# Kernel optimization log

Hardware: AMD Instinct MI355X
Metric: run time of the kernel (lower is better)

The kernel has to match this reference:

```python
import jax, jax.numpy as jnp
import numpy as np
import math

N_NODES = 50000
N_EDGES = 800000
IN_DIM = 128
HID = 128
OUT_DIM = 2048
N_LABEL_EDGES = 4096
POOL_RATIO = 0.5
NUM_HEADS = 8


def seg_sum(x, idx, n):
    return jax.ops.segment_sum(x, idx, num_segments=n)


def graph_conv(x, W, b, src, dst, emask, n):
    # DGL GraphConv, norm='both': D_out^-1/2 A D_in^-1/2 (x W) + b (masked edges)
    deg_out = seg_sum(emask, src, n)
    deg_in = seg_sum(emask, dst, n)
    ns = jax.lax.rsqrt(jnp.maximum(deg_out, 1.0))
    nd = jax.lax.rsqrt(jnp.maximum(deg_in, 1.0))
    h = x @ W
    msg = (h * ns[:, None])[src] * emask[:, None]
    agg = seg_sum(msg, dst, n)
    return agg * nd[:, None] + b


def conv_pool_block(x, src, dst, emask, cW, cb, sW, sb):
    # GraphConv -> ReLU -> SAGPool(top-k by GraphConv score, tanh gate) -> avg||max readout
    n = x.shape[0]
    h = jax.nn.relu(graph_conv(x, cW, cb, src, dst, emask, n))
    score = graph_conv(h, sW, sb, src, dst, emask, n)[:, 0]
    k = int(math.ceil(POOL_RATIO * n))  # static
    _, perm = jax.lax.top_k(score, k)
    h_new = h[perm] * jnp.tanh(score[perm])[:, None]
    # remap edges to the pooled node set; drop edges touching removed nodes via mask
    newid = jnp.full((n,), -1, jnp.int32).at[perm].set(jnp.arange(k, dtype=jnp.int32))
    nsrc = newid[src]
    ndst = newid[dst]
    new_mask = emask * (nsrc >= 0).astype(emask.dtype) * (ndst >= 0).astype(emask.dtype)
    nsrc = jnp.maximum(nsrc, 0)
    ndst = jnp.maximum(ndst, 0)
    readout = jnp.concatenate([h_new.mean(0), h_new.max(0)])[None, :]  # [1, 2*HID]
    return h_new, nsrc, ndst, new_mask, readout


def gat_conv(x, fcW, al, ar, lsrc, ldst, n, slope=0.2):
    # GATConv(1 -> 1, num_heads=8): head feature dim is 1
    h = x @ fcW                      # [n, heads]
    el = h * al
    er = h * ar
    e = jax.nn.leaky_relu(el[lsrc] + er[ldst], slope)  # [E_l, heads]
    emax = jax.ops.segment_max(e, ldst, num_segments=n)
    emax = jnp.where(jnp.isfinite(emax), emax, 0.0)
    ex = jnp.exp(e - emax[ldst])
    denom = seg_sum(ex, ldst, n)
    alpha = ex / jnp.maximum(denom[ldst], 1e-9)
    out = seg_sum(alpha * h[lsrc], ldst, n)            # [n, heads]
    return out[:, :, None]                             # [n, heads, 1]


def setup_inputs() -> dict:
    key = jax.random.key(0)
    ks = jax.random.split(key, 32)

    def rn(k, shape, s=0.05):
        return jax.random.normal(k, shape, jnp.float32) * s

    inp = {}
    inp['feat'] = jax.random.normal(ks[0], (N_NODES, IN_DIM), jnp.float32)
    inp['sequence_feature'] = jax.random.normal(ks[1], (1, 1024), jnp.float32)
    inp['src'] = jax.random.randint(ks[2], (N_EDGES,), 0, N_NODES, jnp.int32)
    inp['dst'] = jax.random.randint(ks[3], (N_EDGES,), 0, N_NODES, jnp.int32)
    inp['label_src'] = jax.random.randint(ks[4], (N_LABEL_EDGES,), 0, OUT_DIM, jnp.int32)
    inp['label_dst'] = jax.random.randint(ks[5], (N_LABEL_EDGES,), 0, OUT_DIM, jnp.int32)
    i = 6
    for b in range(3):
        din = IN_DIM if b == 0 else HID
        inp['cW%d' % b] = rn(ks[i], (din, HID)); i += 1
        inp['cb%d' % b] = jnp.zeros((HID,), jnp.float32)
        inp['sW%d' % b] = rn(ks[i], (HID, 1)); i += 1
        inp['sb%d' % b] = jnp.zeros((1,), jnp.float32)
    inp['lin1W'] = rn(ks[i], (2 * HID + 1024, 2 * HID)); i += 1
    inp['lin1b'] = jnp.zeros((2 * HID,), jnp.float32)
    inp['lin2W'] = rn(ks[i], (2 * HID, HID)); i += 1
    inp['lin2b'] = jnp.zeros((HID,), jnp.float32)
    inp['lin3W'] = rn(ks[i], (HID, OUT_DIM)); i += 1
    inp['lin3b'] = jnp.zeros((OUT_DIM,), jnp.float32)
    inp['gat_fcW'] = rn(ks[i], (1, NUM_HEADS)); i += 1
    inp['gat_al'] = rn(ks[i], (NUM_HEADS,)); i += 1
    inp['gat_ar'] = rn(ks[i], (NUM_HEADS,)); i += 1
    return inp


def reference(feat, sequence_feature, src, dst, label_src, label_dst,
              cW0, cb0, sW0, sb0, cW1, cb1, sW1, sb1, cW2, cb2, sW2, sb2,
              lin1W, lin1b, lin2W, lin2b, lin3W, lin3b,
              gat_fcW, gat_al, gat_ar):
    x, s, d = feat, src, dst
    emask = jnp.ones((src.shape[0],), jnp.float32)
    final = None
    for cW, cb, sW, sb in ((cW0, cb0, sW0, sb0), (cW1, cb1, sW1, sb1), (cW2, cb2, sW2, sb2)):
        x, s, d, emask, ro = conv_pool_block(x, s, d, emask, cW, cb, sW, sb)
        final = ro if final is None else final + ro
    final = jnp.concatenate([final, sequence_feature], axis=-1)  # [1, 2*HID+1024]
    f = jax.nn.relu(final @ lin1W + lin1b)
    # dropout: eval mode -> identity
    f = jax.nn.relu(f @ lin2W + lin2b)
    f = f @ lin3W + lin3b          # [1, OUT_DIM]
    ft = f.T                       # [OUT_DIM, 1]
    gat_out = gat_conv(ft, gat_fcW, gat_al, gat_ar, label_src, label_dst, OUT_DIM)
    max_value = jnp.max(gat_out, axis=1)      # [OUT_DIM, 1]
    _ = ft - jax.nn.relu(max_value)           # computed then discarded, as in source
    return ft.T
```

## Files before the change

kernel.cpp:

```cpp
#include <hip/hip_runtime.h>
#include <hip/hip_bf16.h>
#include <cmath>

#define N0 50000
#define NEDGE 800000
#define NEG_HUGE -3.402823466e38f
#define BMAX 64
#define STRIDE 128

typedef int i32x4 __attribute__((ext_vector_type(4)));
typedef __attribute__((ext_vector_type(8))) short short8v;
typedef __attribute__((ext_vector_type(4))) float f32x4;

__device__ inline float b2f(unsigned short u) { return __uint_as_float(((unsigned)u) << 16); }

__device__ inline unsigned short f2b(float f) {
    __hip_bfloat16 h = __float2bfloat16(f);
    return *(unsigned short*)&h;
}

__device__ inline unsigned fkey(float f) {
    unsigned b = __float_as_uint(f);
    if (b == 0x80000000u) b = 0u;
    return (b & 0x80000000u) ? ~b : (b | 0x80000000u);
}

__device__ inline void atomicMaxF(float* a, float v) {
    if (v >= 0.f) atomicMax((int*)a, __float_as_int(v));
    else          atomicMin((unsigned int*)a, __float_as_uint(v));
}

__global__ void k_init(float* finalv, float* f1raw, int* deg_out, int* fill,
                       int* binsA, int* binsB, float* maxbuf, int* ctrl) {
    int i = blockIdx.x * blockDim.x + threadIdx.x;
    if (i < 256) { finalv[i] = 0.f; f1raw[i] = 0.f; }
    if (i < 384) maxbuf[i] = NEG_HUGE;
    if (i < N0) { deg_out[i] = 0; fill[i] = 0; }
    if (i < 65536) { binsA[i] = 0; binsB[i] = 0; }
    if (i < 2) ctrl[8 + i] = 0;
}

__global__ __launch_bounds__(256) void k_build(
        const int* __restrict__ esrc, const int* __restrict__ edst,
        int* deg_out, int* fill, int* csr_src) {
    int t = blockIdx.x * 256 + threadIdx.x;
    int e0 = t * 4;
    if (e0 >= NEDGE) return;
    i32x4 a = __builtin_nontemporal_load((const i32x4*)(esrc + e0));
    i32x4 bq = __builtin_nontemporal_load((const i32x4*)(edst + e0));
    int s[4] = {a.x, a.y, a.z, a.w};
    int d[4] = {bq.x, bq.y, bq.z, bq.w};
#pragma unroll
    for (int kq = 0; kq < 4; ++kq) {
        atomicAdd(&deg_out[s[kq]], 1);
        int pos = atomicAdd(&fill[d[kq]], 1);
        if (pos < STRIDE) csr_src[(size_t)d[kq] * STRIDE + pos] = s[kq];
    }
}

__global__ __launch_bounds__(256) void k_rmbuild(
        const int* __restrict__ esrc, const int* __restrict__ edst,
        const int2* __restrict__ ein, int use_pair,
        const int* __restrict__ ctrl, int slot,
        const int* __restrict__ newid,
        int2* __restrict__ eout, int* __restrict__ outcnt,
        int* deg_out, int* fill, int* csr_src) {
    __shared__ int wbase[4];
    __shared__ int blkbase;
    int E = (slot < 0) ? NEDGE : ctrl[slot];
    if (blockIdx.x * 256 >= E) return;
    int i = blockIdx.x * 256 + threadIdx.x;
    int lane = threadIdx.x & 63, w = threadIdx.x >> 6;
    int ns = -1, nd = -1;
    if (i < E) {
        int s, d;
        if (use_pair) { int2 pr = ein[i]; s = pr.x; d = pr.y; }
        else { s = esrc[i]; d = edst[i]; }
        ns = newid[s]; nd = newid[d];
    }
    bool keep = (ns >= 0) && (nd >= 0);
    unsigned long long m = __ballot(keep);
    int rank = __popcll(m & ((1ull << lane) - 1ull));
    if (lane == 0) wbase[w] = __popcll(m);
    __syncthreads();
    if (threadIdx.x == 0)
        blkbase = atomicAdd(outcnt, wbase[0] + wbase[1] + wbase[2] + wbase[3]);
    __syncthreads();
    int base = blkbase;
    for (int q = 0; q < w; ++q) base += wbase[q];
    if (keep) {
        eout[base + rank] = make_int2(ns, nd);
        atomicAdd(&deg_out[ns], 1);
        int pos = atomicAdd(&fill[nd], 1);
        if (pos < STRIDE) csr_src[(size_t)nd * STRIDE + pos] = ns;
    }
}

__global__ __launch_bounds__(256) void k_gemm(
        const float* __restrict__ feat, const float* __restrict__ xprev,
        const int* __restrict__ oldid, const float* __restrict__ garr,
        const int* __restrict__ deg_out,
        const float* __restrict__ W, unsigned short* __restrict__ hpre,
        int n, int nprev, int mode) {
    __shared__ short Wt[128][136];
    __shared__ short Xt[64][136];
    __shared__ int ridx_s[64];
    __shared__ float esc_s[64];
    int tid = threadIdx.x;
    int r0 = blockIdx.x * 64;
    if (tid < 64) {
        int gr = r0 + tid;
        int ridx = 0; float esc = 0.f;
        if (gr < n) {
            if (mode == 0) {
                ridx = gr;
                esc = rsqrtf(fmaxf((float)deg_out[gr], 1.f));
            } else {
                int orow = oldid[gr];
                if ((unsigned)orow < (unsigned)nprev) {
                    ridx = orow;
                    esc = rsqrtf(fmaxf((float)deg_out[gr], 1.f)) * garr[gr];
                }
            }
        }
        ridx_s[tid] = ridx;
        esc_s[tid] = esc;
    }
    __syncthreads();
    {
        int col = tid & 127;
        int kh = tid >> 7;
#pragma unroll
        for (int c8 = 0; c8 < 8; ++c8) {
            int kb = kh * 64 + c8 * 8;
            unsigned short v[8];
#pragma unroll
            for (int j = 0; j < 8; ++j)
                v[j] = f2b(W[(size_t)(kb + j) * 128 + col]);
            *(uint4*)&Wt[col][kb] = *(uint4*)v;
        }
    }
    {
        const float* xsrc = (mode == 0) ? feat : xprev;
        int rr = tid >> 2;
        int kx = (tid & 3) * 32;
        const float4* xp = (const float4*)(xsrc + (size_t)ridx_s[rr] * 128 + kx);
#pragma unroll
        for (int c4 = 0; c4 < 8; ++c4) {
            float4 v = xp[c4];
            unsigned short u[4];
            u[0] = f2b(v.x); u[1] = f2b(v.y); u[2] = f2b(v.z); u[3] = f2b(v.w);
            *(uint2*)&Xt[rr][kx + c4 * 4] = *(uint2*)u;
        }
    }
    __syncthreads();

    int lane = tid & 63, w = tid >> 6;
    int row16 = lane & 15;
    int ko = (lane >> 4) * 8;
    f32x4 acc[8];
#pragma unroll
    for (int t = 0; t < 8; ++t) acc[t] = (f32x4){0.f, 0.f, 0.f, 0.f};
#pragma unroll
    for (int kc = 0; kc < 4; ++kc) {
        int kbase = kc * 32 + ko;
        short8v a = *(short8v*)&Xt[w * 16 + row16][kbase];
#pragma unroll
        for (int t = 0; t < 8; ++t) {
            short8v b = *(short8v*)&Wt[t * 16 + row16][kbase];
            acc[t] = __builtin_amdgcn_mfma_f32_16x16x32_bf16(a, b, acc[t], 0, 0, 0);
        }
    }
    int rq = (lane >> 4) * 4;
    float esc[4];
#pragma unroll
    for (int r = 0; r < 4; ++r) esc[r] = esc_s[w * 16 + rq + r];
#pragma unroll
    for (int r = 0; r < 4; ++r) {
        int gr = r0 + w * 16 + rq + r;
        if (gr < n) {
            unsigned short* op = hpre + (size_t)gr * 128;
#pragma unroll
            for (int t = 0; t < 8; ++t)
                op[t * 16 + (lane & 15)] = f2b(acc[t][r] * esc[r]);
        }
    }
}

__global__ __launch_bounds__(256) void k_agg_conv(
        const unsigned short* __restrict__ hpre, const int* __restrict__ fill,
        const int* __restrict__ deg_out,
        const int* __restrict__ csr_src,
        const float* __restrict__ cb, const float* __restrict__ sW,
        float* __restrict__ hpost, float* __restrict__ hs, int n) {
    int wid = threadIdx.x >> 6;
    int lane = threadIdx.x & 63;
    int d = blockIdx.x * 4 + wid;
    if (d >= n) return;
    int degin = fill[d];
    int cnt = min(degin, STRIDE);
    const int* bp = csr_src + (size_t)d * STRIDE;
    float a0 = 0.f, a1 = 0.f;
    int j = 0;
    for (; j + 8 <= cnt; j += 8) {
        int4 s0 = *(const int4*)(bp + j);
        int4 s1 = *(const int4*)(bp + j + 4);
        ushort2 u0 = ((const ushort2*)(hpre + (size_t)s0.x * 128))[lane];
        ushort2 u1 = ((const ushort2*)(hpre + (size_t)s0.y * 128))[lane];
        ushort2 u2 = ((const ushort2*)(hpre + (size_t)s0.z * 128))[lane];
        ushort2 u3 = ((const ushort2*)(hpre + (size_t)s0.w * 128))[lane];
        ushort2 u4 = ((const ushort2*)(hpre + (size_t)s1.x * 128))[lane];
        ushort2 u5 = ((const ushort2*)(hpre + (size_t)s1.y * 128))[lane];
        ushort2 u6 = ((const ushort2*)(hpre + (size_t)s1.z * 128))[lane];
        ushort2 u7 = ((const ushort2*)(hpre + (size_t)s1.w * 128))[lane];
        a0 += ((b2f(u0.x) + b2f(u1.x)) + (b2f(u2.x) + b2f(u3.x))) +
              ((b2f(u4.x) + b2f(u5.x)) + (b2f(u6.x) + b2f(u7.x)));
        a1 += ((b2f(u0.y) + b2f(u1.y)) + (b2f(u2.y) + b2f(u3.y))) +
              ((b2f(u4.y) + b2f(u5.y)) + (b2f(u6.y) + b2f(u7.y)));
    }
    for (; j + 4 <= cnt; j += 4) {
        int4 ss = *(const int4*)(bp + j);
        ushort2 u0 = ((const ushort2*)(hpre + (size_t)ss.x * 128))[lane];
        ushort2 u1 = ((const ushort2*)(hpre + (size_t)ss.y * 128))[lane];
        ushort2 u2 = ((const ushort2*)(hpre + (size_t)ss.z * 128))[lane];
        ushort2 u3 = ((const ushort2*)(hpre + (size_t)ss.w * 128))[lane];
        a0 += (b2f(u0.x) + b2f(u1.x)) + (b2f(u2.x) + b2f(u3.x));
        a1 += (b2f(u0.y) + b2f(u1.y)) + (b2f(u2.y) + b2f(u3.y));
    }
    for (; j < cnt; ++j) {
        int s0 = bp[j];
        ushort2 u0 = ((const ushort2*)(hpre + (size_t)s0 * 128))[lane];
        a0 += b2f(u0.x);
        a1 += b2f(u0.y);
    }
    float nd2 = rsqrtf(fmaxf((float)degin, 1.f));
    int c0 = lane * 2;
    float h0 = fmaxf(fmaf(a0, nd2, cb[c0]), 0.f);
    float h1 = fmaxf(fmaf(a1, nd2, cb[c0 + 1]), 0.f);
    ((float2*)(hpost + (size_t)d * 128))[lane] = make_float2(h0, h1);
    float v = h0 * sW[c0] + h1 * sW[c0 + 1];
#pragma unroll
    for (int off = 32; off; off >>= 1) v += __shfl_down(v, off);
    if (lane == 0) hs[d] = v * rsqrtf(fmaxf((float)deg_out[d], 1.f));
}

__global__ void k_score_hist(const float* __restrict__ hs, const int* __restrict__ fill,
                             const int* __restrict__ csr_src,
                             const float* __restrict__ sb, float* score,
                             int* binsA, int n) {
    int d = blockIdx.x * blockDim.x + threadIdx.x;
    if (d >= n) return;
    int degin = fill[d];
    int cnt = min(degin, STRIDE);
    const int* bp = csr_src + (size_t)d * STRIDE;
    float sum = 0.f;
    int j = 0;
    for (; j + 8 <= cnt; j += 8) {
        int4 s0 = *(const int4*)(bp + j);
        int4 s1 = *(const int4*)(bp + j + 4);
        sum += ((hs[s0.x] + hs[s0.y]) + (hs[s0.z] + hs[s0.w])) +
               ((hs[s1.x] + hs[s1.y]) + (hs[s1.z] + hs[s1.w]));
    }
    for (; j + 4 <= cnt; j += 4) {
        int4 ss = *(const int4*)(bp + j);
        sum += (hs[ss.x] + hs[ss.y]) + (hs[ss.z] + hs[ss.w]);
    }
    for (; j < cnt; ++j) sum += hs[bp[j]];
    float sc = rsqrtf(fmaxf((float)degin, 1.f)) * sum + sb[0];
    score[d] = sc;
    atomicAdd(&binsA[fkey(sc) >> 16], 1);
}

__global__ void k_rhist2(const float* __restrict__ score, const int* __restrict__ ctrl,
                         int n, int* binsB) {
    unsigned p16 = (unsigned)ctrl[3];
    for (int i = blockIdx.x * 256 + threadIdx.x; i < n; i += gridDim.x * 256) {
        unsigned u = fkey(score[i]);
        if ((u >> 16) == p16) atomicAdd(&binsB[u & 0xFFFFu], 1);
    }
}

__global__ void k_rpick(int stage, int k0, int* ctrl, const int* __restrict__ bins) {
    __shared__ int gs[64];
    __shared__ int arr[1024];
    __shared__ int wsum[16];
    __shared__ int sChunk, sKrem;
    int t = threadIdx.x;
    {
        int c = t >> 4, sub = t & 15;
        const int4* p4 = (const int4*)(bins + (size_t)c * 1024);
        int s = 0;
#pragma unroll
        for (int q = 0; q < 16; ++q) {
            int4 v = p4[q * 16 + sub];
            s += v.x + v.y + v.z + v.w;
        }
#pragma unroll
        for (int off = 8; off; off >>= 1) s += __shfl_down(s, off, 16);
        if (sub == 0) gs[c] = s;
    }
    __syncthreads();
    if (t == 0) {
        int kneed = (stage == 0) ? k0 : ctrl[4];
        int cum = 0, c = 63;
        for (; c >= 1; --c) { int v = gs[c]; if (cum + v >= kneed) break; cum += v; }
        sChunk = c; sKrem = kneed - cum;
    }
    __syncthreads();
    int c = sChunk;
    int v = bins[(size_t)c * 1024 + t];
    arr[t] = v;
    int lane = t & 63, w = t >> 6;
    int s = v;
#pragma unroll
    for (int off = 32; off; off >>= 1) s += __shfl_down(s, off);
    if (lane == 0) wsum[w] = s;
    __syncthreads();
    if (t == 0) {
        int kneed = sKrem;
        int cum = 0, w2 = 15;
        for (; w2 >= 1; --w2) { int vv = wsum[w2]; if (cum + vv >= kneed) break; cum += vv; }
        int j = 63;
        for (; j >= 1; --j) { int vv = arr[w2 * 64 + j]; if (cum + vv >= kneed) break; cum += vv; }
        int bin = c * 1024 + w2 * 64 + j;
        if (stage == 0) { ctrl[3] = bin; ctrl[4] = kneed - cum; }
        else {
            ctrl[0] = (int)((((unsigned)ctrl[3]) << 16) | (unsigned)bin);
            ctrl[2] = kneed - cum;
        }
    }
}

__global__ void k_ccnt(const float* __restrict__ score, const int* __restrict__ ctrl,
                       int n, int* cntG, int* cntE) {
    __shared__ int wG[16], wE[16];
    int b = blockIdx.x;
    int i = b * 1024 + threadIdx.x;
    int lane = threadIdx.x & 63, wid = threadIdx.x >> 6;
    unsigned T = (unsigned)ctrl[0];
    bool inb = (i < n);
    unsigned u = inb ? fkey(score[i]) : 0u;
    bool isG = inb && (u > T);
    bool isE = inb && (u == T);
    unsigned long long mG = __ballot(isG);
    unsigned long long mE = __ballot(isE);
    if (lane == 0) { wG[wid] = __popcll(mG); wE[wid] = __popcll(mE); }
    __syncthreads();
    if (threadIdx.x == 0) {
        int sg = 0, se = 0;
#pragma unroll
        for (int w = 0; w < 16; ++w) { sg += wG[w]; se += wE[w]; }
        cntG[b] = sg; cntE[b] = se;
    }
}

__global__ void k_cemit(const float* __restrict__ score, const int* __restrict__ ctrl,
                        const int* __restrict__ cntG, const int* __restrict__ cntE,
                        int n, int knext, int* newid, int* oldid, float* garr,
                        int* deg_out, int* fill, int* binsA, int* binsB) {
    __shared__ int wG[16], wE[16];
    __shared__ int sGoff, sEoff;
    int b = blockIdx.x;
    int i = b * 1024 + threadIdx.x;
    if (knext > 0) {
        for (int z = i; z < 65536; z += gridDim.x * 1024) { binsA[z] = 0; binsB[z] = 0; }
        if (i < knext) { deg_out[i] = 0; fill[i] = 0; }
    }
    int lane = threadIdx.x & 63, wid = threadIdx.x >> 6;
    unsigned T = (unsigned)ctrl[0];
    int needEq = ctrl[2];
    bool inb = (i < n);
    float sc = inb ? score[i] : 0.f;
    unsigned u = inb ? fkey(sc) : 0u;
    bool isG = inb && (u > T);
    bool isE = inb && (u == T);
    unsigned long long mG = __ballot(isG);
    unsigned long long mE = __ballot(isE);
    if (lane == 0) { wG[wid] = __popcll(mG); wE[wid] = __popcll(mE); }
    if (threadIdx.x < 64) {
        int l = threadIdx.x;
        int vg = (l < b) ? cntG[l] : 0;
        int ve = (l < b) ? cntE[l] : 0;
#pragma unroll
        for (int off2 = 32; off2; off2 >>= 1) {
            vg += __shfl_down(vg, off2);
            ve += __shfl_down(ve, off2);
        }
        if (l == 0) { sGoff = vg; sEoff = ve; }
    }
    __syncthreads();
    unsigned long long below = (1ull << lane) - 1ull;
    int gW = 0, eW = 0;
    for (int w = 0; w < wid; ++w) { gW += wG[w]; eW += wE[w]; }
    int Gb = sGoff + gW + __popcll(mG & below);
    int Eb = sEoff + eW + __popcll(mE & below);
    if (inb) {
        bool sel = isG || (isE && (Eb < needEq));
        if (sel) {
            int j = Gb + min(Eb, needEq);
            newid[i] = j;
            oldid[j] = i;
            garr[j] = tanhf(sc);
        } else {
            newid[i] = -1;
        }
    }
}

__global__ void k_readout(const float* __restrict__ hpost, const int* __restrict__ oldid,
                          const float* __restrict__ garr, float* finalv, float* maxbuf,
                          int k, int n, float invk) {
    int c = threadIdx.x;
    float sum = 0.f, mx = NEG_HUGE;
    for (int r = blockIdx.x; r < k; r += gridDim.x) {
        int o = oldid[r];
        if ((unsigned)o >= (unsigned)n) continue;
        float g = garr[r];
        float v = hpost[(size_t)o * 128 + c] * g;
        sum += v;
        mx = fmaxf(mx, v);
    }
    atomicAdd(&finalv[c], sum * invk);
    atomicMaxF(&maxbuf[c], mx);
}

__global__ void k_mlp1(const float* __restrict__ finalv, const float* __restrict__ maxbuf,
                       const float* __restrict__ seq, const float* __restrict__ W1,
                       float* f1raw) {
    int o = threadIdx.x;
    int j0 = blockIdx.x * 128;
    float acc = 0.f;
    for (int jj = 0; jj < 128; ++jj) {
        int j = j0 + jj;
        float fv;
        if (j < 128) fv = finalv[j];
        else if (j < 256) fv = maxbuf[j - 128] + maxbuf[j] + maxbuf[j + 128];
        else fv = seq[j - 256];
        acc = fmaf(fv, W1[(size_t)j * 256 + o], acc);
    }
    atomicAdd(&f1raw[o], acc);
}

__global__ void k_mlp2(const float* __restrict__ f1raw, const float* __restrict__ b1,
                       const float* __restrict__ W2, const float* __restrict__ bb2,
                       float* f2v) {
    __shared__ float f1s[256];
    int t = threadIdx.x;
    f1s[t] = fmaxf(f1raw[t] + b1[t], 0.f);
    f1s[t + 128] = fmaxf(f1raw[t + 128] + b1[t + 128], 0.f);
    __syncthreads();
    float acc = 0.f;
    for (int j = 0; j < 256; ++j)
        acc = fmaf(f1s[j], W2[(size_t)j * 128 + t], acc);
    f2v[t] = fmaxf(acc + bb2[t], 0.f);
}

__global__ void k_mlp3(const float* __restrict__ f2v, const float* __restrict__ W3,
                       const float* __restrict__ b3, float* out) {
    __shared__ float f2s[128];
    int t = threadIdx.x;
    f2s[t] = f2v[t];
    __syncthreads();
    int col = blockIdx.x * 128 + t;
    float acc = 0.f;
    for (int j = 0; j < 128; ++j)
        acc = fmaf(f2s[j], W3[(size_t)j * 2048 + col], acc);
    out[col] = acc + b3[col];
}

extern "C" void kernel_launch(void* const* d_in, const int* in_sizes, int n_in,
                              void* d_out, int out_size, void* d_ws, size_t ws_size,
                              hipStream_t stream) {
    (void)in_sizes; (void)n_in; (void)out_size; (void)ws_size;
    const float* feat = (const float*)d_in[0];
    const float* seq  = (const float*)d_in[1];
    const int* src = (const int*)d_in[2];
    const int* dst = (const int*)d_in[3];
    const float *cW[3], *cb[3], *sW[3], *sb[3];
    for (int b = 0; b < 3; ++b) {
        cW[b] = (const float*)d_in[6 + 4 * b];
        cb[b] = (const float*)d_in[7 + 4 * b];
        sW[b] = (const float*)d_in[8 + 4 * b];
        sb[b] = (const float*)d_in[9 + 4 * b];
    }
    const float* lin1W = (const float*)d_in[18];
    const float* lin1b = (const float*)d_in[19];
    const float* lin2W = (const float*)d_in[20];
    const float* lin2b = (const float*)d_in[21];
    const float* lin3W = (const float*)d_in[22];
    const float* lin3b = (const float*)d_in[23];
    float* out = (float*)d_out;

    char* p = (char*)d_ws;
    size_t off = 0;
    auto alloc = [&](size_t bytes) -> void* {
        void* r = p + off;
        off = (off + bytes + 255) & ~(size_t)255;
        return r;
    };
    unsigned short* hpre = (unsigned short*)alloc((size_t)N0 * 128 * 2);
    float* hpost  = (float*)alloc((size_t)N0 * 128 * 4);
    float* hs     = (float*)alloc((size_t)N0 * 4);
    float* score  = (float*)alloc((size_t)N0 * 4);
    int* deg_out  = (int*)alloc((size_t)N0 * 4);
    int* fill     = (int*)alloc((size_t)N0 * 4);
    int2* epair1  = (int2*)alloc((size_t)NEDGE * 8);
    int* csr_src  = (int*)alloc((size_t)N0 * STRIDE * 4);
    int* newid    = (int*)alloc((size_t)N0 * 4);
    int* oldid    = (int*)alloc((size_t)25000 * 4);
    float* garr   = (float*)alloc((size_t)25000 * 4);
    float* maxbuf = (float*)alloc(3 * 128 * 4);
    float* finalv = (float*)alloc(256 * 4);
    float* f1raw  = (float*)alloc(256 * 4);
    float* f2v    = (float*)alloc(128 * 4);
    int* ctrl     = (int*)alloc(64 * 4);
    int* binsA    = (int*)alloc(65536 * 4);
    int* binsB    = (int*)alloc(65536 * 4);
    int* cntG     = (int*)alloc(BMAX * 4);
    int* cntE     = (int*)alloc(BMAX * 4);
    int2* epair2  = (int2*)hpre;

    const int nb[3] = {50000, 25000, 12500};
    const int kb[3] = {25000, 12500, 6250};

    k_init<<<256, 256, 0, stream>>>(finalv, f1raw, deg_out, fill, binsA, binsB,
                                    maxbuf, ctrl);

    for (int b = 0; b < 3; ++b) {
        int n = nb[b], k = kb[b];
        int B = (n + 1023) / 1024;
        if (b == 0)
            k_build<<<(NEDGE / 4 + 255) / 256, 256, 0, stream>>>(src, dst, deg_out, fill,
                                                                 csr_src);
        else if (b == 1)
            k_rmbuild<<<(NEDGE + 255) / 256, 256, 0, stream>>>(
                src, dst, (const int2*)0, 0, ctrl, -1, newid, epair1, ctrl + 8,
                deg_out, fill, csr_src);
        else
            k_rmbuild<<<(NEDGE + 255) / 256, 256, 0, stream>>>(
                (const int*)0, (const int*)0, epair1, 1, ctrl, 8, newid, epair2, ctrl + 9,
                deg_out, fill, csr_src);
        k_gemm<<<(n + 63) / 64, 256, 0, stream>>>(feat, hpost, oldid, garr, deg_out, cW[b],
                                                  hpre, n, (b > 0) ? nb[b - 1] : 1,
                                                  (b == 0) ? 0 : 1);
        k_agg_conv<<<(n + 3) / 4, 256, 0, stream>>>(hpre, fill, deg_out, csr_src, cb[b],
                                                    sW[b], hpost, hs, n);
        k_score_hist<<<(n + 255) / 256, 256, 0, stream>>>(hs, fill, csr_src, sb[b],
                                                          score, binsA, n);
        k_rpick<<<1, 1024, 0, stream>>>(0, k, ctrl, binsA);
        k_rhist2<<<128, 256, 0, stream>>>(score, ctrl, n, binsB);
        k_rpick<<<1, 1024, 0, stream>>>(1, k, ctrl, binsB);
        k_ccnt<<<B, 1024, 0, stream>>>(score, ctrl, n, cntG, cntE);
        k_cemit<<<B, 1024, 0, stream>>>(score, ctrl, cntG, cntE, n, (b < 2) ? kb[b] : 0,
                                        newid, oldid, garr, deg_out, fill, binsA, binsB);
        k_readout<<<512, 128, 0, stream>>>(hpost, oldid, garr, finalv, maxbuf + b * 128,
                                           k, n, 1.0f / (float)k);
    }

    k_mlp1<<<10, 256, 0, stream>>>(finalv, maxbuf, seq, lin1W, f1raw);
    k_mlp2<<<1, 128, 0, stream>>>(f1raw, lin1b, lin2W, lin2b, f2v);
    k_mlp3<<<16, 128, 0, stream>>>(f2v, lin3W, lin3b, out);
}
```

Measured before the change: 586.1 us.

## Fuse top-k count, emit and readout into one kernel; merge MLP kernels

```diff
diff --git a/kernel.cpp b/kernel.cpp
--- a/kernel.cpp
+++ b/kernel.cpp
@@ -5,7 +5,6 @@
 #define N0 50000
 #define NEDGE 800000
 #define NEG_HUGE -3.402823466e38f
-#define BMAX 64
 #define STRIDE 128
 
 typedef int i32x4 __attribute__((ext_vector_type(4)));
@@ -30,10 +29,10 @@
     else          atomicMin((unsigned int*)a, __float_as_uint(v));
 }
 
-__global__ void k_init(float* finalv, float* f1raw, int* deg_out, int* fill,
+__global__ void k_init(float* finalv, int* deg_out, int* fill,
                        int* binsA, int* binsB, float* maxbuf, int* ctrl) {
     int i = blockIdx.x * blockDim.x + threadIdx.x;
-    if (i < 256) { finalv[i] = 0.f; f1raw[i] = 0.f; }
+    if (i < 256) finalv[i] = 0.f;
     if (i < 384) maxbuf[i] = NEG_HUGE;
     if (i < N0) { deg_out[i] = 0; fill[i] = 0; }
     if (i < 65536) { binsA[i] = 0; binsB[i] = 0; }
@@ -331,44 +330,44 @@
     }
 }
 
-__global__ void k_ccnt(const float* __restrict__ score, const int* __restrict__ ctrl,
-                       int n, int* cntG, int* cntE) {
+__global__ __launch_bounds__(1024) void k_cemit2(
+        const float* __restrict__ score, const int* __restrict__ ctrl,
+        int n, int knext, int* newid, int* oldid, float* garr,
+        int* deg_out, int* fill, int* binsA, int* binsB,
+        const float* __restrict__ hpost, float* finalv, float* maxbuf, float invk) {
     __shared__ int wG[16], wE[16];
-    int b = blockIdx.x;
-    int i = b * 1024 + threadIdx.x;
-    int lane = threadIdx.x & 63, wid = threadIdx.x >> 6;
-    unsigned T = (unsigned)ctrl[0];
-    bool inb = (i < n);
-    unsigned u = inb ? fkey(score[i]) : 0u;
-    bool isG = inb && (u > T);
-    bool isE = inb && (u == T);
-    unsigned long long mG = __ballot(isG);
-    unsigned long long mE = __ballot(isE);
-    if (lane == 0) { wG[wid] = __popcll(mG); wE[wid] = __popcll(mE); }
-    __syncthreads();
-    if (threadIdx.x == 0) {
-        int sg = 0, se = 0;
-#pragma unroll
-        for (int w = 0; w < 16; ++w) { sg += wG[w]; se += wE[w]; }
-        cntG[b] = sg; cntE[b] = se;
-    }
-}
-
-__global__ void k_cemit(const float* __restrict__ score, const int* __restrict__ ctrl,
-                        const int* __restrict__ cntG, const int* __restrict__ cntE,
-                        int n, int knext, int* newid, int* oldid, float* garr,
-                        int* deg_out, int* fill, int* binsA, int* binsB) {
-    __shared__ int wG[16], wE[16];
-    __shared__ int sGoff, sEoff;
-    int b = blockIdx.x;
-    int i = b * 1024 + threadIdx.x;
-    if (knext > 0) {
-        for (int z = i; z < 65536; z += gridDim.x * 1024) { binsA[z] = 0; binsB[z] = 0; }
-        if (i < knext) { deg_out[i] = 0; fill[i] = 0; }
-    }
-    int lane = threadIdx.x & 63, wid = threadIdx.x >> 6;
+    __shared__ int redCG[16], redCE[16];
+    __shared__ int selIdx[1024];
+    __shared__ float selG[1024];
+    __shared__ int selCnt;
+    __shared__ float redS[1024], redM[1024];
+    int b = blockIdx.x, tid = threadIdx.x;
+    int lane = tid & 63, wv = tid >> 6;
     unsigned T = (unsigned)ctrl[0];
     int needEq = ctrl[2];
+
+    if (knext > 0) {
+        int gt = b * 1024 + tid, nt = gridDim.x * 1024;
+        for (int z = gt; z < 65536; z += nt) { binsA[z] = 0; binsB[z] = 0; }
+        for (int z = gt; z < knext; z += nt) { deg_out[z] = 0; fill[z] = 0; }
+    }
+
+    int cg_ = 0, ce_ = 0;
+    int end = b << 10;
+    for (int i = tid; i < end; i += 1024) {
+        unsigned u = fkey(score[i]);
+        cg_ += (u > T);
+        ce_ += (u == T);
+    }
+#pragma unroll
+    for (int off = 32; off; off >>= 1) {
+        cg_ += __shfl_down(cg_, off);
+        ce_ += __shfl_down(ce_, off);
+    }
+    if (lane == 0) { redCG[wv] = cg_; redCE[wv] = ce_; }
+    if (tid == 0) selCnt = 0;
+
+    int i = (b << 10) + tid;
     bool inb = (i < n);
     float sc = inb ? score[i] : 0.f;
     unsigned u = inb ? fkey(sc) : 0u;
@@ -376,22 +375,15 @@
     bool isE = inb && (u == T);
     unsigned long long mG = __ballot(isG);
     unsigned long long mE = __ballot(isE);
-    if (lane == 0) { wG[wid] = __popcll(mG); wE[wid] = __popcll(mE); }
-    if (threadIdx.x < 64) {
-        int l = threadIdx.x;
-        int vg = (l < b) ? cntG[l] : 0;
-        int ve = (l < b) ? cntE[l] : 0;
-#pragma unroll
-        for (int off2 = 32; off2; off2 >>= 1) {
-            vg += __shfl_down(vg, off2);
-            ve += __shfl_down(ve, off2);
-        }
-        if (l == 0) { sGoff = vg; sEoff = ve; }
-    }
-    __syncthreads();
+    if (lane == 0) { wG[wv] = __popcll(mG); wE[wv] = __popcll(mE); }
+    __syncthreads();
+
+    int sGoff = 0, sEoff = 0;
+#pragma unroll
+    for (int w = 0; w < 16; ++w) { sGoff += redCG[w]; sEoff += redCE[w]; }
+    int gW = 0, eW = 0;
+    for (int w = 0; w < wv; ++w) { gW += wG[w]; eW += wE[w]; }
     unsigned long long below = (1ull << lane) - 1ull;
-    int gW = 0, eW = 0;
-    for (int w = 0; w < wid; ++w) { gW += wG[w]; eW += wE[w]; }
     int Gb = sGoff + gW + __popcll(mG & below);
     int Eb = sEoff + eW + __popcll(mE & below);
     if (inb) {
@@ -400,72 +392,95 @@
             int j = Gb + min(Eb, needEq);
             newid[i] = j;
             oldid[j] = i;
-            garr[j] = tanhf(sc);
+            float g = tanhf(sc);
+            garr[j] = g;
+            int p = atomicAdd(&selCnt, 1);
+            selIdx[p] = i;
+            selG[p] = g;
         } else {
             newid[i] = -1;
         }
     }
-}
-
-__global__ void k_readout(const float* __restrict__ hpost, const int* __restrict__ oldid,
-                          const float* __restrict__ garr, float* finalv, float* maxbuf,
-                          int k, int n, float invk) {
-    int c = threadIdx.x;
+    __syncthreads();
+
+    int m = selCnt;
+    int grp = tid >> 7, c = tid & 127;
     float sum = 0.f, mx = NEG_HUGE;
-    for (int r = blockIdx.x; r < k; r += gridDim.x) {
-        int o = oldid[r];
-        if ((unsigned)o >= (unsigned)n) continue;
-        float g = garr[r];
-        float v = hpost[(size_t)o * 128 + c] * g;
+    for (int r = grp; r < m; r += 8) {
+        float v = hpost[(size_t)selIdx[r] * 128 + c] * selG[r];
         sum += v;
         mx = fmaxf(mx, v);
     }
-    atomicAdd(&finalv[c], sum * invk);
-    atomicMaxF(&maxbuf[c], mx);
-}
-
-__global__ void k_mlp1(const float* __restrict__ finalv, const float* __restrict__ maxbuf,
-                       const float* __restrict__ seq, const float* __restrict__ W1,
-                       float* f1raw) {
-    int o = threadIdx.x;
-    int j0 = blockIdx.x * 128;
-    float acc = 0.f;
-    for (int jj = 0; jj < 128; ++jj) {
-        int j = j0 + jj;
-        float fv;
-        if (j < 128) fv = finalv[j];
-        else if (j < 256) fv = maxbuf[j - 128] + maxbuf[j] + maxbuf[j + 128];
-        else fv = seq[j - 256];
-        acc = fmaf(fv, W1[(size_t)j * 256 + o], acc);
-    }
-    atomicAdd(&f1raw[o], acc);
-}
-
-__global__ void k_mlp2(const float* __restrict__ f1raw, const float* __restrict__ b1,
-                       const float* __restrict__ W2, const float* __restrict__ bb2,
-                       float* f2v) {
+    redS[tid] = sum;
+    redM[tid] = mx;
+    __syncthreads();
+    if (tid < 128) {
+        float s2 = 0.f, m2 = NEG_HUGE;
+#pragma unroll
+        for (int g2 = 0; g2 < 8; ++g2) {
+            s2 += redS[g2 * 128 + tid];
+            m2 = fmaxf(m2, redM[g2 * 128 + tid]);
+        }
+        atomicAdd(&finalv[tid], s2 * invk);
+        atomicMaxF(&maxbuf[tid], m2);
+    }
+}
+
+__global__ __launch_bounds__(1024) void k_mlp(
+        const float* __restrict__ finalv, const float* __restrict__ maxbuf,
+        const float* __restrict__ seq,
+        const float* __restrict__ W1, const float* __restrict__ b1,
+        const float* __restrict__ W2, const float* __restrict__ b2,
+        const float* __restrict__ W3, const float* __restrict__ b3,
+        float* out) {
+    __shared__ float fv[1280];
+    __shared__ float part[1024];
     __shared__ float f1s[256];
-    int t = threadIdx.x;
-    f1s[t] = fmaxf(f1raw[t] + b1[t], 0.f);
-    f1s[t + 128] = fmaxf(f1raw[t + 128] + b1[t + 128], 0.f);
-    __syncthreads();
-    float acc = 0.f;
-    for (int j = 0; j < 256; ++j)
-        acc = fmaf(f1s[j], W2[(size_t)j * 128 + t], acc);
-    f2v[t] = fmaxf(acc + bb2[t], 0.f);
-}
-
-__global__ void k_mlp3(const float* __restrict__ f2v, const float* __restrict__ W3,
-                       const float* __restrict__ b3, float* out) {
     __shared__ float f2s[128];
-    int t = threadIdx.x;
-    f2s[t] = f2v[t];
-    __syncthreads();
-    int col = blockIdx.x * 128 + t;
-    float acc = 0.f;
-    for (int j = 0; j < 128; ++j)
-        acc = fmaf(f2s[j], W3[(size_t)j * 2048 + col], acc);
-    out[col] = acc + b3[col];
+    int tid = threadIdx.x;
+    for (int j = tid; j < 1280; j += 1024) {
+        float v;
+        if (j < 128) v = finalv[j];
+        else if (j < 256) v = maxbuf[j - 128] + maxbuf[j] + maxbuf[j + 128];
+        else v = seq[j - 256];
+        fv[j] = v;
+    }
+    __syncthreads();
+    {
+        int o = tid & 255, pr = tid >> 8;
+        float acc = 0.f;
+        for (int j = pr * 320; j < (pr + 1) * 320; ++j)
+            acc = fmaf(fv[j], W1[(size_t)j * 256 + o], acc);
+        part[tid] = acc;
+    }
+    __syncthreads();
+    if (tid < 256) {
+        float a = part[tid] + part[tid + 256] + part[tid + 512] + part[tid + 768];
+        f1s[tid] = fmaxf(a + b1[tid], 0.f);
+    }
+    __syncthreads();
+    {
+        int o = tid & 127, pr = tid >> 7;
+        float acc = 0.f;
+        for (int j = pr * 32; j < (pr + 1) * 32; ++j)
+            acc = fmaf(f1s[j], W2[(size_t)j * 128 + o], acc);
+        part[tid] = acc;
+    }
+    __syncthreads();
+    if (tid < 128) {
+        float a = 0.f;
+#pragma unroll
+        for (int q = 0; q < 8; ++q) a += part[q * 128 + tid];
+        f2s[tid] = fmaxf(a + b2[tid], 0.f);
+    }
+    __syncthreads();
+    for (int col = tid; col < 2048; col += 1024) {
+        float acc = 0.f;
+#pragma unroll 4
+        for (int j = 0; j < 128; ++j)
+            acc = fmaf(f2s[j], W3[(size_t)j * 2048 + col], acc);
+        out[col] = acc + b3[col];
+    }
 }
 
 extern "C" void kernel_launch(void* const* d_in, const int* in_sizes, int n_in,
@@ -511,20 +526,15 @@
     float* garr   = (float*)alloc((size_t)25000 * 4);
     float* maxbuf = (float*)alloc(3 * 128 * 4);
     float* finalv = (float*)alloc(256 * 4);
-    float* f1raw  = (float*)alloc(256 * 4);
-    float* f2v    = (float*)alloc(128 * 4);
     int* ctrl     = (int*)alloc(64 * 4);
     int* binsA    = (int*)alloc(65536 * 4);
     int* binsB    = (int*)alloc(65536 * 4);
-    int* cntG     = (int*)alloc(BMAX * 4);
-    int* cntE     = (int*)alloc(BMAX * 4);
     int2* epair2  = (int2*)hpre;
 
     const int nb[3] = {50000, 25000, 12500};
     const int kb[3] = {25000, 12500, 6250};
 
-    k_init<<<256, 256, 0, stream>>>(finalv, f1raw, deg_out, fill, binsA, binsB,
-                                    maxbuf, ctrl);
+    k_init<<<256, 256, 0, stream>>>(finalv, deg_out, fill, binsA, binsB, maxbuf, ctrl);
 
     for (int b = 0; b < 3; ++b) {
         int n = nb[b], k = kb[b];
@@ -550,14 +560,12 @@
         k_rpick<<<1, 1024, 0, stream>>>(0, k, ctrl, binsA);
         k_rhist2<<<128, 256, 0, stream>>>(score, ctrl, n, binsB);
         k_rpick<<<1, 1024, 0, stream>>>(1, k, ctrl, binsB);
-        k_ccnt<<<B, 1024, 0, stream>>>(score, ctrl, n, cntG, cntE);
-        k_cemit<<<B, 1024, 0, stream>>>(score, ctrl, cntG, cntE, n, (b < 2) ? kb[b] : 0,
-                                        newid, oldid, garr, deg_out, fill, binsA, binsB);
-        k_readout<<<512, 128, 0, stream>>>(hpost, oldid, garr, finalv, maxbuf + b * 128,
-                                           k, n, 1.0f / (float)k);
-    }
-
-    k_mlp1<<<10, 256, 0, stream>>>(finalv, maxbuf, seq, lin1W, f1raw);
-    k_mlp2<<<1, 128, 0, stream>>>(f1raw, lin1b, lin2W, lin2b, f2v);
-    k_mlp3<<<16, 128, 0, stream>>>(f2v, lin3W, lin3b, out);
-}
+        k_cemit2<<<B, 1024, 0, stream>>>(score, ctrl, n, (b < 2) ? kb[b] : 0,
+                                         newid, oldid, garr, deg_out, fill, binsA, binsB,
+                                         hpost, finalv, maxbuf + b * 128,
+                                         1.0f / (float)k);
+    }
+
+    k_mlp<<<1, 1024, 0, stream>>>(finalv, maxbuf, seq, lin1W, lin1b, lin2W, lin2b,
+                                  lin3W, lin3b, out);
+}
```

Result: no change. 597.4 us (+1.9%).
